# Optimization experiments

Hardware: AMD Instinct MI355X
Metric: run time of the kernel (lower is better)

Reference implementation:

```python
import jax, jax.numpy as jnp
import numpy as np

B, N, E = 32, 2000, 32000      # graphs, nodes/graph, edges/graph
V, D, R, K = 100000, 128, 39, 8  # vocab, emb_dim, n_relation, n_bases
EPS = 1e-5


def setup_inputs() -> dict:
    key = jax.random.key(0)
    ks = jax.random.split(key, 8)
    node_ids = jax.random.randint(ks[0], (B, N), 0, V)
    edge_index = jax.random.randint(ks[1], (B, 2, E), 0, N)
    edge_type = jax.random.randint(ks[2], (B, E), 0, R)
    embedding = jax.random.normal(ks[3], (V, D), jnp.float32) * D ** -0.5
    bases = jax.random.normal(ks[4], (K, D, D), jnp.float32) * D ** -0.5
    comp = jax.random.normal(ks[5], (R, K), jnp.float32) * K ** -0.5
    root = jax.random.normal(ks[6], (D, D), jnp.float32) * D ** -0.5
    bias = jnp.zeros((D,), jnp.float32)
    return dict(node_ids=node_ids, edge_index=edge_index, edge_type=edge_type,
                embedding=embedding, bases=bases, comp=comp, root=root, bias=bias)


def _graph_fwd(node_ids, edge_index, edge_type, embedding, bases, comp, root, bias):
    # RGCNConv with basis decomposition and per-relation MEAN aggregation (PyG default).
    x = embedding[node_ids]                       # [N, D] per-graph node features
    src, dst = edge_index[0], edge_index[1]       # j -> i, aggregate at dst
    x_src = x[src]                                # [E, D]
    # mean normalizer per (dst, relation) bucket
    comb = dst * R + edge_type                    # [E]
    cnt = jax.ops.segment_sum(jnp.ones((E,), jnp.float32), comb, num_segments=N * R)
    inv = jnp.where(cnt > 0, 1.0 / cnt, 0.0)[comb]  # [E]
    # W_r = sum_k comp[r,k] * bases[k]; fold comp coefficients + mean norm into edge weights
    w = comp[edge_type] * inv[:, None]            # [E, K]
    out = x @ root + bias                         # root/self connection
    for k in range(K):                            # small fixed loop over bases
        zk = jax.ops.segment_sum(w[:, k:k + 1] * x_src, dst, num_segments=N)  # [N, D]
        out = out + zk @ bases[k]
    g = out.sum(axis=0)                           # sum pool over nodes
    # torch.nn.functional.normalize(p=2, eps=1e-5)
    return g / jnp.maximum(jnp.linalg.norm(g), EPS)


def reference(node_ids, edge_index, edge_type, embedding, bases, comp, root, bias):
    f = jax.vmap(_graph_fwd, in_axes=(0, 0, 0, None, None, None, None, None))
    return f(node_ids, edge_index, edge_type, embedding, bases, comp, root, bias)  # [B, D]
```

## Files before the change

kernel.cpp:

```cpp
#include <hip/hip_runtime.h>
#include <math.h>

#define Bn 32
#define Nn 2000
#define En 32000
#define Vn 100000
#define Dn 128
#define Rn 39
#define Kn 8

#define SUBS 8
#define NPS (Nn / SUBS)
#define WPG 128
#define EQ (En / 4)


__global__ __launch_bounds__(1024) void cntinv_kernel(const int* __restrict__ edge_index,
                                                      const int* __restrict__ edge_type,
                                                      float* __restrict__ inv) {
    int b = blockIdx.x, sub = blockIdx.y;
    int s0 = sub * NPS;
    __shared__ int loc[NPS * Rn];
    for (int i = threadIdx.x; i < NPS * Rn; i += 1024) loc[i] = 0;
    __syncthreads();
    const int4* dst4 = (const int4*)(edge_index + (b * 2 + 1) * En);
    const int4* et4  = (const int4*)(edge_type + b * En);
    for (int q = threadIdx.x; q < EQ; q += 1024) {
        int4 d = dst4[q];
        int4 t = et4[q];
        int x;
        x = d.x - s0; if ((unsigned)x < NPS) atomicAdd(&loc[x * Rn + t.x], 1);
        x = d.y - s0; if ((unsigned)x < NPS) atomicAdd(&loc[x * Rn + t.y], 1);
        x = d.z - s0; if ((unsigned)x < NPS) atomicAdd(&loc[x * Rn + t.z], 1);
        x = d.w - s0; if ((unsigned)x < NPS) atomicAdd(&loc[x * Rn + t.w], 1);
    }
    __syncthreads();
    float* ivb = inv + (size_t)b * En;
    for (int q = threadIdx.x; q < EQ; q += 1024) {
        int4 d = dst4[q];
        int4 t = et4[q];
        int e = 4 * q, x;
        x = d.x - s0; if ((unsigned)x < NPS) ivb[e]     = 1.0f / (float)loc[x * Rn + t.x];
        x = d.y - s0; if ((unsigned)x < NPS) ivb[e + 1] = 1.0f / (float)loc[x * Rn + t.y];
        x = d.z - s0; if ((unsigned)x < NPS) ivb[e + 2] = 1.0f / (float)loc[x * Rn + t.z];
        x = d.w - s0; if ((unsigned)x < NPS) ivb[e + 3] = 1.0f / (float)loc[x * Rn + t.w];
    }
}

__global__ __launch_bounds__(1024) void a_kernel(const int* __restrict__ edge_index,
                                                 const int* __restrict__ edge_type,
                                                 const float* __restrict__ inv,
                                                 const float* __restrict__ comp,
                                                 float* __restrict__ a) {
    int b = blockIdx.x, sub = blockIdx.y;
    int s0 = sub * NPS;
    __shared__ float s[NPS * Rn];
    __shared__ float comp_l[Rn * Kn];
    for (int i = threadIdx.x; i < NPS * Rn; i += 1024) s[i] = 0.0f;
    if (threadIdx.x < Rn * Kn) comp_l[threadIdx.x] = comp[threadIdx.x];
    __syncthreads();
    const int4*   src4 = (const int4*)(edge_index + (b * 2 + 0) * En);
    const int4*   et4  = (const int4*)(edge_type + b * En);
    const float4* iv4  = (const float4*)(inv + (size_t)b * En);
    for (int q = threadIdx.x; q < EQ; q += 1024) {
        int4 sv = src4[q];
        int4 tv = et4[q];
        float4 iv = iv4[q];
        int x;
        x = sv.x - s0; if ((unsigned)x < NPS) atomicAdd(&s[x * Rn + tv.x], iv.x);
        x = sv.y - s0; if ((unsigned)x < NPS) atomicAdd(&s[x * Rn + tv.y], iv.y);
        x = sv.z - s0; if ((unsigned)x < NPS) atomicAdd(&s[x * Rn + tv.z], iv.z);
        x = sv.w - s0; if ((unsigned)x < NPS) atomicAdd(&s[x * Rn + tv.w], iv.w);
    }
    __syncthreads();
    float* g = a + ((size_t)b * Nn + s0) * Kn;
    for (int i = threadIdx.x; i < NPS * Kn; i += 1024) {
        int n = i >> 3, k = i & 7;
        float acc = 0.0f;
        const float* srow = &s[n * Rn];
        for (int t = 0; t < Rn; t++) acc += srow[t] * comp_l[t * Kn + k];
        g[i] = acc;
    }
}

__global__ __launch_bounds__(256) void gather_kernel(const int* __restrict__ node_ids,
                                                     const float* __restrict__ emb,
                                                     const float* __restrict__ a,
                                                     float* __restrict__ partial) {
    int b = blockIdx.x;
    int lane = threadIdx.x & 63, wv = threadIdx.x >> 6;
    int W = blockIdx.y * 4 + wv;
    float acc[18];
#pragma unroll
    for (int k = 0; k < 18; k++) acc[k] = 0.0f;
    const int*   nb = node_ids + b * Nn;
    const float* ab = a + (size_t)b * Nn * Kn;
    for (int n0 = W; n0 < Nn; n0 += 4 * WPG) {
        bool   has[4];
        int    nn[4];
        float2 v[4];
        float4 a0[4], a1[4];
#pragma unroll
        for (int i = 0; i < 4; i++) {
            int n = n0 + i * WPG;
            has[i] = n < Nn;
            nn[i]  = has[i] ? n : n0;
        }
#pragma unroll
        for (int i = 0; i < 4; i++) {
            int nid = nb[nn[i]];
            v[i] = has[i] ? ((const float2*)(emb + (size_t)nid * Dn))[lane]
                          : make_float2(0.f, 0.f);
            const float4* ar = (const float4*)(ab + (size_t)nn[i] * Kn);
            a0[i] = ar[0]; a1[i] = ar[1];
        }
#pragma unroll
        for (int i = 0; i < 4; i++) {
            float w[9] = {a0[i].x, a0[i].y, a0[i].z, a0[i].w,
                          a1[i].x, a1[i].y, a1[i].z, a1[i].w, 1.0f};
#pragma unroll
            for (int k = 0; k < 9; k++) {
                acc[2 * k]     += w[k] * v[i].x;
                acc[2 * k + 1] += w[k] * v[i].y;
            }
        }
    }
    float2* gp = (float2*)(partial + ((size_t)b * WPG + W) * 9 * Dn);
#pragma unroll
    for (int k = 0; k < 9; k++)
        gp[k * 64 + lane] = make_float2(acc[2 * k], acc[2 * k + 1]);
}

__global__ __launch_bounds__(256) void matvec_kernel(const float* __restrict__ partial,
                                                     const float* __restrict__ root,
                                                     const float* __restrict__ bases,
                                                     float* __restrict__ gmat) {
    int b = blockIdx.x, m = blockIdx.y;
    int d = threadIdx.x & (Dn - 1), h = threadIdx.x >> 7;
    __shared__ float ts[Dn];
    __shared__ float tsh[2][Dn];
    const float* p = partial + (size_t)b * WPG * 9 * Dn + m * Dn + d;
    float s0 = 0.f, s1 = 0.f, s2 = 0.f, s3 = 0.f;
    for (int c = h; c < WPG; c += 8) {
        s0 += p[(size_t)(c    ) * 9 * Dn];
        s1 += p[(size_t)(c + 2) * 9 * Dn];
        s2 += p[(size_t)(c + 4) * 9 * Dn];
        s3 += p[(size_t)(c + 6) * 9 * Dn];
    }
    tsh[h][d] = (s0 + s1) + (s2 + s3);
    __syncthreads();
    if (h == 0) ts[d] = tsh[0][d] + tsh[1][d];
    __syncthreads();
    const float* M = (m == 8) ? root : bases + (size_t)m * Dn * Dn;
    float g = 0.0f;
    for (int j = h * 64; j < h * 64 + 64; j++) g += ts[j] * M[j * Dn + d];
    __syncthreads();
    tsh[h][d] = g;
    __syncthreads();
    if (h == 0) gmat[((size_t)b * 9 + m) * Dn + d] = tsh[0][d] + tsh[1][d];
}

__global__ __launch_bounds__(128) void norm_kernel(const float* __restrict__ gmat,
                                                   const float* __restrict__ bias,
                                                   float* __restrict__ out) {
    int b = blockIdx.x, d = threadIdx.x;
    float g = (float)Nn * bias[d];
    const float* gb = gmat + (size_t)b * 9 * Dn + d;
#pragma unroll
    for (int m = 0; m < 9; m++) g += gb[m * Dn];
    float ss = g * g;
#pragma unroll
    for (int off = 32; off > 0; off >>= 1) ss += __shfl_down(ss, off, 64);
    __shared__ float s2[2];
    if ((threadIdx.x & 63) == 0) s2[threadIdx.x >> 6] = ss;
    __syncthreads();
    float nrm = sqrtf(s2[0] + s2[1]);
    out[b * Dn + d] = g / fmaxf(nrm, 1e-5f);
}

extern "C" void kernel_launch(void* const* d_in, const int* in_sizes, int n_in,
                              void* d_out, int out_size, void* d_ws, size_t ws_size,
                              hipStream_t stream) {
    const int*   node_ids   = (const int*)d_in[0];
    const int*   edge_index = (const int*)d_in[1];
    const int*   edge_type  = (const int*)d_in[2];
    const float* embedding  = (const float*)d_in[3];
    const float* bases      = (const float*)d_in[4];
    const float* comp       = (const float*)d_in[5];
    const float* root       = (const float*)d_in[6];
    const float* bias       = (const float*)d_in[7];
    float*       out        = (float*)d_out;

    char* w = (char*)d_ws;
    float* inv     = (float*)(w + 0);
    float* a       = (float*)(w + 4096000);
    float* partial = (float*)(w + 6144000);
    float* gmat    = (float*)(w + 25018368);

    cntinv_kernel<<<dim3(Bn, SUBS),    1024, 0, stream>>>(edge_index, edge_type, inv);
    a_kernel     <<<dim3(Bn, SUBS),    1024, 0, stream>>>(edge_index, edge_type, inv, comp, a);
    gather_kernel<<<dim3(Bn, WPG / 4), 256,  0, stream>>>(node_ids, embedding, a, partial);
    matvec_kernel<<<dim3(Bn, 9),       256,  0, stream>>>(partial, root, bases, gmat);
    norm_kernel  <<<Bn, 128, 0, stream>>>(gmat, bias, out);
}
```

Measured before the change: 156.1 us.

## Fuse gather, matvec and normalize into one kernel with last-block ticket reduction

Merges the gather, matvec and norm kernels into a single kernel. Each block first reduces its 16 waves' partial sums in shared memory, then writes one partial per block. A per-graph atomic ticket elects the last block to finish, and that block does the cross-block reduction, the 9 matvecs against bases/root and the L2 normalization. This removes two kernel launches and most of the partial-buffer traffic. In exchange, the final matvec runs on only 32 blocks (one per graph) instead of 288, which serializes that stage, and correctness now depends on threadfence ordering and the ticket reset done in a_kernel.

```diff
diff --git a/kernel.cpp b/kernel.cpp
--- a/kernel.cpp
+++ b/kernel.cpp
@@ -11,24 +11,25 @@
 
 #define SUBS 8
 #define NPS (Nn / SUBS)
-#define WPG 128
 #define EQ (En / 4)
-
-
-__global__ __launch_bounds__(1024) void cntinv_kernel(const int* __restrict__ edge_index,
-                                                      const int* __restrict__ edge_type,
-                                                      float* __restrict__ inv) {
+#define GB 8
+#define GW 16
+#define WPG (GB * GW)
+#define TPB 1024
+
+
+__global__ __launch_bounds__(TPB) void cntinv_kernel(const int* __restrict__ edge_index,
+                                                     const int* __restrict__ edge_type,
+                                                     float* __restrict__ inv) {
     int b = blockIdx.x, sub = blockIdx.y;
     int s0 = sub * NPS;
     __shared__ int loc[NPS * Rn];
-    for (int i = threadIdx.x; i < NPS * Rn; i += 1024) loc[i] = 0;
+    for (int i = threadIdx.x; i < NPS * Rn; i += TPB) loc[i] = 0;
     __syncthreads();
     const int4* dst4 = (const int4*)(edge_index + (b * 2 + 1) * En);
     const int4* et4  = (const int4*)(edge_type + b * En);
-    for (int q = threadIdx.x; q < EQ; q += 1024) {
-        int4 d = dst4[q];
-        int4 t = et4[q];
-        int x;
+    for (int q = threadIdx.x; q < EQ; q += TPB) {
+        int4 d = dst4[q]; int4 t = et4[q]; int x;
         x = d.x - s0; if ((unsigned)x < NPS) atomicAdd(&loc[x * Rn + t.x], 1);
         x = d.y - s0; if ((unsigned)x < NPS) atomicAdd(&loc[x * Rn + t.y], 1);
         x = d.z - s0; if ((unsigned)x < NPS) atomicAdd(&loc[x * Rn + t.z], 1);
@@ -36,9 +37,8 @@
     }
     __syncthreads();
     float* ivb = inv + (size_t)b * En;
-    for (int q = threadIdx.x; q < EQ; q += 1024) {
-        int4 d = dst4[q];
-        int4 t = et4[q];
+    for (int q = threadIdx.x; q < EQ; q += TPB) {
+        int4 d = dst4[q]; int4 t = et4[q];
         int e = 4 * q, x;
         x = d.x - s0; if ((unsigned)x < NPS) ivb[e]     = 1.0f / (float)loc[x * Rn + t.x];
         x = d.y - s0; if ((unsigned)x < NPS) ivb[e + 1] = 1.0f / (float)loc[x * Rn + t.y];
@@ -47,26 +47,25 @@
     }
 }
 
-__global__ __launch_bounds__(1024) void a_kernel(const int* __restrict__ edge_index,
-                                                 const int* __restrict__ edge_type,
-                                                 const float* __restrict__ inv,
-                                                 const float* __restrict__ comp,
-                                                 float* __restrict__ a) {
+__global__ __launch_bounds__(TPB) void a_kernel(const int* __restrict__ edge_index,
+                                                const int* __restrict__ edge_type,
+                                                const float* __restrict__ inv,
+                                                const float* __restrict__ comp,
+                                                float* __restrict__ a,
+                                                int* __restrict__ ticket) {
     int b = blockIdx.x, sub = blockIdx.y;
+    if (sub == 0 && threadIdx.x == 0) ticket[b] = 0;
     int s0 = sub * NPS;
     __shared__ float s[NPS * Rn];
     __shared__ float comp_l[Rn * Kn];
-    for (int i = threadIdx.x; i < NPS * Rn; i += 1024) s[i] = 0.0f;
+    for (int i = threadIdx.x; i < NPS * Rn; i += TPB) s[i] = 0.0f;
     if (threadIdx.x < Rn * Kn) comp_l[threadIdx.x] = comp[threadIdx.x];
     __syncthreads();
     const int4*   src4 = (const int4*)(edge_index + (b * 2 + 0) * En);
     const int4*   et4  = (const int4*)(edge_type + b * En);
     const float4* iv4  = (const float4*)(inv + (size_t)b * En);
-    for (int q = threadIdx.x; q < EQ; q += 1024) {
-        int4 sv = src4[q];
-        int4 tv = et4[q];
-        float4 iv = iv4[q];
-        int x;
+    for (int q = threadIdx.x; q < EQ; q += TPB) {
+        int4 sv = src4[q]; int4 tv = et4[q]; float4 iv = iv4[q]; int x;
         x = sv.x - s0; if ((unsigned)x < NPS) atomicAdd(&s[x * Rn + tv.x], iv.x);
         x = sv.y - s0; if ((unsigned)x < NPS) atomicAdd(&s[x * Rn + tv.y], iv.y);
         x = sv.z - s0; if ((unsigned)x < NPS) atomicAdd(&s[x * Rn + tv.z], iv.z);
@@ -74,7 +73,7 @@
     }
     __syncthreads();
     float* g = a + ((size_t)b * Nn + s0) * Kn;
-    for (int i = threadIdx.x; i < NPS * Kn; i += 1024) {
+    for (int i = threadIdx.x; i < NPS * Kn; i += TPB) {
         int n = i >> 3, k = i & 7;
         float acc = 0.0f;
         const float* srow = &s[n * Rn];
@@ -83,13 +82,18 @@
     }
 }
 
-__global__ __launch_bounds__(256) void gather_kernel(const int* __restrict__ node_ids,
-                                                     const float* __restrict__ emb,
-                                                     const float* __restrict__ a,
-                                                     float* __restrict__ partial) {
-    int b = blockIdx.x;
-    int lane = threadIdx.x & 63, wv = threadIdx.x >> 6;
-    int W = blockIdx.y * 4 + wv;
+__global__ __launch_bounds__(TPB) void gather_final_kernel(
+    const int* __restrict__ node_ids, const float* __restrict__ emb,
+    const float* __restrict__ a, const float* __restrict__ root,
+    const float* __restrict__ bases, const float* __restrict__ bias,
+    float* partial, int* ticket, float* __restrict__ out)
+{
+    __shared__ float red[GW * 9 * Dn];
+    __shared__ int isLast;
+    int b = blockIdx.x, sub = blockIdx.y;
+    int tid = threadIdx.x, lane = tid & 63, wv = tid >> 6;
+    int W = sub * GW + wv;
+
     float acc[18];
 #pragma unroll
     for (int k = 0; k < 18; k++) acc[k] = 0.0f;
@@ -125,57 +129,64 @@
             }
         }
     }
-    float2* gp = (float2*)(partial + ((size_t)b * WPG + W) * 9 * Dn);
 #pragma unroll
     for (int k = 0; k < 9; k++)
-        gp[k * 64 + lane] = make_float2(acc[2 * k], acc[2 * k + 1]);
-}
-
-__global__ __launch_bounds__(256) void matvec_kernel(const float* __restrict__ partial,
-                                                     const float* __restrict__ root,
-                                                     const float* __restrict__ bases,
-                                                     float* __restrict__ gmat) {
-    int b = blockIdx.x, m = blockIdx.y;
-    int d = threadIdx.x & (Dn - 1), h = threadIdx.x >> 7;
-    __shared__ float ts[Dn];
-    __shared__ float tsh[2][Dn];
-    const float* p = partial + (size_t)b * WPG * 9 * Dn + m * Dn + d;
-    float s0 = 0.f, s1 = 0.f, s2 = 0.f, s3 = 0.f;
-    for (int c = h; c < WPG; c += 8) {
-        s0 += p[(size_t)(c    ) * 9 * Dn];
-        s1 += p[(size_t)(c + 2) * 9 * Dn];
-        s2 += p[(size_t)(c + 4) * 9 * Dn];
-        s3 += p[(size_t)(c + 6) * 9 * Dn];
-    }
-    tsh[h][d] = (s0 + s1) + (s2 + s3);
-    __syncthreads();
-    if (h == 0) ts[d] = tsh[0][d] + tsh[1][d];
-    __syncthreads();
-    const float* M = (m == 8) ? root : bases + (size_t)m * Dn * Dn;
+        ((float2*)&red[(wv * 9 + k) * Dn])[lane] = make_float2(acc[2 * k], acc[2 * k + 1]);
+    __syncthreads();
+
+    float* gp = partial + ((size_t)(b * GB + sub)) * 9 * Dn;
+    for (int i = tid; i < 9 * Dn; i += TPB) {
+        float s = 0.0f;
+#pragma unroll
+        for (int w = 0; w < GW; w++) s += red[w * 9 * Dn + i];
+        gp[i] = s;
+    }
+    __threadfence();
+    if (tid == 0) {
+        int old = atomicAdd(&ticket[b], 1);
+        isLast = ((old & (GB - 1)) == (GB - 1));
+    }
+    __syncthreads();
+    if (!isLast) return;
+    __threadfence();
+
+    volatile const float* pb = partial + (size_t)b * GB * 9 * Dn;
+    for (int i = tid; i < 9 * Dn; i += TPB) {
+        float s = 0.0f;
+#pragma unroll
+        for (int c = 0; c < GB; c++) s += pb[c * 9 * Dn + i];
+        red[i] = s;
+    }
+    __syncthreads();
+
+    for (int u = tid; u < 9 * Dn; u += TPB) {
+        int m = u >> 7, d = u & (Dn - 1);
+        const float* M  = (m == 8) ? root : bases + (size_t)m * Dn * Dn;
+        const float* ts = &red[m * Dn];
+        float g = 0.0f;
+        for (int j = 0; j < Dn; j++) g += ts[j] * M[j * Dn + d];
+        red[9 * Dn + u] = g;
+    }
+    __syncthreads();
+
     float g = 0.0f;
-    for (int j = h * 64; j < h * 64 + 64; j++) g += ts[j] * M[j * Dn + d];
-    __syncthreads();
-    tsh[h][d] = g;
-    __syncthreads();
-    if (h == 0) gmat[((size_t)b * 9 + m) * Dn + d] = tsh[0][d] + tsh[1][d];
-}
-
-__global__ __launch_bounds__(128) void norm_kernel(const float* __restrict__ gmat,
-                                                   const float* __restrict__ bias,
-                                                   float* __restrict__ out) {
-    int b = blockIdx.x, d = threadIdx.x;
-    float g = (float)Nn * bias[d];
-    const float* gb = gmat + (size_t)b * 9 * Dn + d;
-#pragma unroll
-    for (int m = 0; m < 9; m++) g += gb[m * Dn];
-    float ss = g * g;
-#pragma unroll
-    for (int off = 32; off > 0; off >>= 1) ss += __shfl_down(ss, off, 64);
-    __shared__ float s2[2];
-    if ((threadIdx.x & 63) == 0) s2[threadIdx.x >> 6] = ss;
-    __syncthreads();
-    float nrm = sqrtf(s2[0] + s2[1]);
-    out[b * Dn + d] = g / fmaxf(nrm, 1e-5f);
+    if (tid < Dn) {
+        g = (float)Nn * bias[tid];
+#pragma unroll
+        for (int m = 0; m < 9; m++) g += red[9 * Dn + m * Dn + tid];
+        red[18 * Dn + tid] = g;
+    }
+    float ss = (tid < Dn) ? g * g : 0.0f;
+    if (tid < 128) {
+#pragma unroll
+        for (int off = 32; off > 0; off >>= 1) ss += __shfl_down(ss, off, 64);
+        if ((tid & 63) == 0) red[19 * Dn + (tid >> 6)] = ss;
+    }
+    __syncthreads();
+    if (tid < Dn) {
+        float nrm = sqrtf(red[19 * Dn] + red[19 * Dn + 1]);
+        out[b * Dn + tid] = red[18 * Dn + tid] / fmaxf(nrm, 1e-5f);
+    }
 }
 
 extern "C" void kernel_launch(void* const* d_in, const int* in_sizes, int n_in,
@@ -195,11 +206,10 @@
     float* inv     = (float*)(w + 0);
     float* a       = (float*)(w + 4096000);
     float* partial = (float*)(w + 6144000);
-    float* gmat    = (float*)(w + 25018368);
-
-    cntinv_kernel<<<dim3(Bn, SUBS),    1024, 0, stream>>>(edge_index, edge_type, inv);
-    a_kernel     <<<dim3(Bn, SUBS),    1024, 0, stream>>>(edge_index, edge_type, inv, comp, a);
-    gather_kernel<<<dim3(Bn, WPG / 4), 256,  0, stream>>>(node_ids, embedding, a, partial);
-    matvec_kernel<<<dim3(Bn, 9),       256,  0, stream>>>(partial, root, bases, gmat);
-    norm_kernel  <<<Bn, 128, 0, stream>>>(gmat, bias, out);
-}
+    int*   ticket  = (int*)  (w + 7323648);
+
+    cntinv_kernel      <<<dim3(Bn, SUBS), TPB, 0, stream>>>(edge_index, edge_type, inv);
+    a_kernel           <<<dim3(Bn, SUBS), TPB, 0, stream>>>(edge_index, edge_type, inv, comp, a, ticket);
+    gather_final_kernel<<<dim3(Bn, GB),   TPB, 0, stream>>>(node_ids, embedding, a, root,
+                                                            bases, bias, partial, ticket, out);
+}
```

Result: slower. 226.0 us (+44.7%).

## Fuse per-node weight and gather kernels, fold normalization into matvec

Applied to the files above, without the earlier changes.

Merges the per-node basis-weight computation with the embedding gather, so the weights stay in shared memory and never round-trip through global memory. It also folds the final L2 normalization into the matvec kernel, using a last-block ticket counter per graph. This removes two kernel launches and the global write and read of the weight array. The cost is that the gather now runs on only 256 blocks of 1024 threads instead of 1024 blocks of 256, so it has less parallelism for hiding embedding-load latency. The ticket scheme also relies on threadfence ordering.

```diff
diff --git a/kernel.cpp b/kernel.cpp
--- a/kernel.cpp
+++ b/kernel.cpp
@@ -11,24 +11,24 @@
 
 #define SUBS 8
 #define NPS (Nn / SUBS)
-#define WPG 128
+#define GW 16
+#define WPG (SUBS * GW)
 #define EQ (En / 4)
-
-
-__global__ __launch_bounds__(1024) void cntinv_kernel(const int* __restrict__ edge_index,
-                                                      const int* __restrict__ edge_type,
-                                                      float* __restrict__ inv) {
+#define TPB 1024
+
+
+__global__ __launch_bounds__(TPB) void cntinv_kernel(const int* __restrict__ edge_index,
+                                                     const int* __restrict__ edge_type,
+                                                     float* __restrict__ inv) {
     int b = blockIdx.x, sub = blockIdx.y;
     int s0 = sub * NPS;
     __shared__ int loc[NPS * Rn];
-    for (int i = threadIdx.x; i < NPS * Rn; i += 1024) loc[i] = 0;
+    for (int i = threadIdx.x; i < NPS * Rn; i += TPB) loc[i] = 0;
     __syncthreads();
     const int4* dst4 = (const int4*)(edge_index + (b * 2 + 1) * En);
     const int4* et4  = (const int4*)(edge_type + b * En);
-    for (int q = threadIdx.x; q < EQ; q += 1024) {
-        int4 d = dst4[q];
-        int4 t = et4[q];
-        int x;
+    for (int q = threadIdx.x; q < EQ; q += TPB) {
+        int4 d = dst4[q]; int4 t = et4[q]; int x;
         x = d.x - s0; if ((unsigned)x < NPS) atomicAdd(&loc[x * Rn + t.x], 1);
         x = d.y - s0; if ((unsigned)x < NPS) atomicAdd(&loc[x * Rn + t.y], 1);
         x = d.z - s0; if ((unsigned)x < NPS) atomicAdd(&loc[x * Rn + t.z], 1);
@@ -36,9 +36,8 @@
     }
     __syncthreads();
     float* ivb = inv + (size_t)b * En;
-    for (int q = threadIdx.x; q < EQ; q += 1024) {
-        int4 d = dst4[q];
-        int4 t = et4[q];
+    for (int q = threadIdx.x; q < EQ; q += TPB) {
+        int4 d = dst4[q]; int4 t = et4[q];
         int e = 4 * q, x;
         x = d.x - s0; if ((unsigned)x < NPS) ivb[e]     = 1.0f / (float)loc[x * Rn + t.x];
         x = d.y - s0; if ((unsigned)x < NPS) ivb[e + 1] = 1.0f / (float)loc[x * Rn + t.y];
@@ -47,77 +46,69 @@
     }
 }
 
-__global__ __launch_bounds__(1024) void a_kernel(const int* __restrict__ edge_index,
+__global__ __launch_bounds__(TPB) void ag_kernel(const int* __restrict__ node_ids,
+                                                 const int* __restrict__ edge_index,
                                                  const int* __restrict__ edge_type,
                                                  const float* __restrict__ inv,
                                                  const float* __restrict__ comp,
-                                                 float* __restrict__ a) {
+                                                 const float* __restrict__ emb,
+                                                 float* __restrict__ partial,
+                                                 int* __restrict__ ticket) {
     int b = blockIdx.x, sub = blockIdx.y;
+    int tid = threadIdx.x;
+    if (sub == 0 && tid == 0) ticket[b] = 0;
     int s0 = sub * NPS;
     __shared__ float s[NPS * Rn];
     __shared__ float comp_l[Rn * Kn];
-    for (int i = threadIdx.x; i < NPS * Rn; i += 1024) s[i] = 0.0f;
-    if (threadIdx.x < Rn * Kn) comp_l[threadIdx.x] = comp[threadIdx.x];
+    __shared__ float w_loc[NPS * 9];
+    for (int i = tid; i < NPS * Rn; i += TPB) s[i] = 0.0f;
+    if (tid < Rn * Kn) comp_l[tid] = comp[tid];
     __syncthreads();
     const int4*   src4 = (const int4*)(edge_index + (b * 2 + 0) * En);
     const int4*   et4  = (const int4*)(edge_type + b * En);
     const float4* iv4  = (const float4*)(inv + (size_t)b * En);
-    for (int q = threadIdx.x; q < EQ; q += 1024) {
-        int4 sv = src4[q];
-        int4 tv = et4[q];
-        float4 iv = iv4[q];
-        int x;
+    for (int q = tid; q < EQ; q += TPB) {
+        int4 sv = src4[q]; int4 tv = et4[q]; float4 iv = iv4[q]; int x;
         x = sv.x - s0; if ((unsigned)x < NPS) atomicAdd(&s[x * Rn + tv.x], iv.x);
         x = sv.y - s0; if ((unsigned)x < NPS) atomicAdd(&s[x * Rn + tv.y], iv.y);
         x = sv.z - s0; if ((unsigned)x < NPS) atomicAdd(&s[x * Rn + tv.z], iv.z);
         x = sv.w - s0; if ((unsigned)x < NPS) atomicAdd(&s[x * Rn + tv.w], iv.w);
     }
     __syncthreads();
-    float* g = a + ((size_t)b * Nn + s0) * Kn;
-    for (int i = threadIdx.x; i < NPS * Kn; i += 1024) {
+    for (int i = tid; i < NPS * Kn; i += TPB) {
         int n = i >> 3, k = i & 7;
         float acc = 0.0f;
         const float* srow = &s[n * Rn];
         for (int t = 0; t < Rn; t++) acc += srow[t] * comp_l[t * Kn + k];
-        g[i] = acc;
-    }
-}
-
-__global__ __launch_bounds__(256) void gather_kernel(const int* __restrict__ node_ids,
-                                                     const float* __restrict__ emb,
-                                                     const float* __restrict__ a,
-                                                     float* __restrict__ partial) {
-    int b = blockIdx.x;
-    int lane = threadIdx.x & 63, wv = threadIdx.x >> 6;
-    int W = blockIdx.y * 4 + wv;
+        w_loc[n * 9 + k] = acc;
+    }
+    for (int i = tid; i < NPS; i += TPB) w_loc[i * 9 + 8] = 1.0f;
+    __syncthreads();
+
+    int lane = tid & 63, wv = tid >> 6;
     float acc[18];
 #pragma unroll
     for (int k = 0; k < 18; k++) acc[k] = 0.0f;
-    const int*   nb = node_ids + b * Nn;
-    const float* ab = a + (size_t)b * Nn * Kn;
-    for (int n0 = W; n0 < Nn; n0 += 4 * WPG) {
+    const int* nb = node_ids + b * Nn;
+    for (int l0 = wv; l0 < NPS; l0 += 4 * GW) {
         bool   has[4];
-        int    nn[4];
+        int    ll[4];
         float2 v[4];
-        float4 a0[4], a1[4];
 #pragma unroll
         for (int i = 0; i < 4; i++) {
-            int n = n0 + i * WPG;
-            has[i] = n < Nn;
-            nn[i]  = has[i] ? n : n0;
+            int l = l0 + i * GW;
+            has[i] = l < NPS;
+            ll[i]  = has[i] ? l : l0;
         }
 #pragma unroll
         for (int i = 0; i < 4; i++) {
-            int nid = nb[nn[i]];
+            int nid = nb[s0 + ll[i]];
             v[i] = has[i] ? ((const float2*)(emb + (size_t)nid * Dn))[lane]
                           : make_float2(0.f, 0.f);
-            const float4* ar = (const float4*)(ab + (size_t)nn[i] * Kn);
-            a0[i] = ar[0]; a1[i] = ar[1];
         }
 #pragma unroll
         for (int i = 0; i < 4; i++) {
-            float w[9] = {a0[i].x, a0[i].y, a0[i].z, a0[i].w,
-                          a1[i].x, a1[i].y, a1[i].z, a1[i].w, 1.0f};
+            const float* w = &w_loc[ll[i] * 9];
 #pragma unroll
             for (int k = 0; k < 9; k++) {
                 acc[2 * k]     += w[k] * v[i].x;
@@ -125,20 +116,25 @@
             }
         }
     }
+    int W = sub * GW + wv;
     float2* gp = (float2*)(partial + ((size_t)b * WPG + W) * 9 * Dn);
 #pragma unroll
     for (int k = 0; k < 9; k++)
         gp[k * 64 + lane] = make_float2(acc[2 * k], acc[2 * k + 1]);
 }
 
-__global__ __launch_bounds__(256) void matvec_kernel(const float* __restrict__ partial,
-                                                     const float* __restrict__ root,
-                                                     const float* __restrict__ bases,
-                                                     float* __restrict__ gmat) {
+__global__ __launch_bounds__(256) void mvn_kernel(const float* __restrict__ partial,
+                                                  const float* __restrict__ root,
+                                                  const float* __restrict__ bases,
+                                                  const float* __restrict__ bias,
+                                                  float* gmat,
+                                                  int* ticket,
+                                                  float* __restrict__ out) {
     int b = blockIdx.x, m = blockIdx.y;
     int d = threadIdx.x & (Dn - 1), h = threadIdx.x >> 7;
     __shared__ float ts[Dn];
     __shared__ float tsh[2][Dn];
+    __shared__ int isLast;
     const float* p = partial + (size_t)b * WPG * 9 * Dn + m * Dn + d;
     float s0 = 0.f, s1 = 0.f, s2 = 0.f, s3 = 0.f;
     for (int c = h; c < WPG; c += 8) {
@@ -158,24 +154,32 @@
     tsh[h][d] = g;
     __syncthreads();
     if (h == 0) gmat[((size_t)b * 9 + m) * Dn + d] = tsh[0][d] + tsh[1][d];
-}
-
-__global__ __launch_bounds__(128) void norm_kernel(const float* __restrict__ gmat,
-                                                   const float* __restrict__ bias,
-                                                   float* __restrict__ out) {
-    int b = blockIdx.x, d = threadIdx.x;
-    float g = (float)Nn * bias[d];
-    const float* gb = gmat + (size_t)b * 9 * Dn + d;
-#pragma unroll
-    for (int m = 0; m < 9; m++) g += gb[m * Dn];
-    float ss = g * g;
+    __threadfence();
+    if (threadIdx.x == 0) {
+        int old = atomicAdd(&ticket[b], 1);
+        isLast = ((old % 9) == 8);
+    }
+    __syncthreads();
+    if (!isLast) return;
+    __threadfence();
+
+    float gg = 0.0f;
+    if (threadIdx.x < Dn) {
+        gg = (float)Nn * bias[d];
+        const float* gb = gmat + (size_t)b * 9 * Dn + d;
+#pragma unroll
+        for (int mm = 0; mm < 9; mm++) gg += gb[mm * Dn];
+        ts[d] = gg;
+    }
+    float ss = (threadIdx.x < Dn) ? gg * gg : 0.0f;
 #pragma unroll
     for (int off = 32; off > 0; off >>= 1) ss += __shfl_down(ss, off, 64);
-    __shared__ float s2[2];
-    if ((threadIdx.x & 63) == 0) s2[threadIdx.x >> 6] = ss;
-    __syncthreads();
-    float nrm = sqrtf(s2[0] + s2[1]);
-    out[b * Dn + d] = g / fmaxf(nrm, 1e-5f);
+    if ((threadIdx.x & 63) == 0) tsh[0][threadIdx.x >> 6] = ss;
+    __syncthreads();
+    if (threadIdx.x < Dn) {
+        float nrm = sqrtf(tsh[0][0] + tsh[0][1]);
+        out[b * Dn + d] = ts[d] / fmaxf(nrm, 1e-5f);
+    }
 }
 
 extern "C" void kernel_launch(void* const* d_in, const int* in_sizes, int n_in,
@@ -193,13 +197,13 @@
 
     char* w = (char*)d_ws;
     float* inv     = (float*)(w + 0);
-    float* a       = (float*)(w + 4096000);
-    float* partial = (float*)(w + 6144000);
-    float* gmat    = (float*)(w + 25018368);
-
-    cntinv_kernel<<<dim3(Bn, SUBS),    1024, 0, stream>>>(edge_index, edge_type, inv);
-    a_kernel     <<<dim3(Bn, SUBS),    1024, 0, stream>>>(edge_index, edge_type, inv, comp, a);
-    gather_kernel<<<dim3(Bn, WPG / 4), 256,  0, stream>>>(node_ids, embedding, a, partial);
-    matvec_kernel<<<dim3(Bn, 9),       256,  0, stream>>>(partial, root, bases, gmat);
-    norm_kernel  <<<Bn, 128, 0, stream>>>(gmat, bias, out);
-}
+    float* partial = (float*)(w + 4096000);
+    float* gmat    = (float*)(w + 22970368);
+    int*   ticket  = (int*)  (w + 23117824);
+
+    cntinv_kernel<<<dim3(Bn, SUBS), TPB, 0, stream>>>(edge_index, edge_type, inv);
+    ag_kernel    <<<dim3(Bn, SUBS), TPB, 0, stream>>>(node_ids, edge_index, edge_type,
+                                                      inv, comp, embedding, partial, ticket);
+    mvn_kernel   <<<dim3(Bn, 9),    256, 0, stream>>>(partial, root, bases, bias,
+                                                      gmat, ticket, out);
+}
```

New measurement: 165.7 us. +6.1%, slower.

## Flatten bucket indexing, deepen gather unroll, transpose partial layout for vectorized matvec

Applied to the files above, without the earlier changes.

The count and aggregation kernels now compute a flat (node*R+type) index and test it against a block's contiguous bucket range, replacing the subtract-then-multiply form. The gather loop processes 8 nodes per iteration instead of 4, giving more loads in flight at the cost of more registers. Partial sums are stored as [b][k][wave][D] so the matvec reduction reads contiguous float4 rows, with eight partitions reduced through shared memory. A redundant shared-memory zeroing and an extra barrier were also added.

```diff
diff --git a/kernel.cpp b/kernel.cpp
--- a/kernel.cpp
+++ b/kernel.cpp
@@ -13,37 +13,35 @@
 #define NPS (Nn / SUBS)
 #define WPG 128
 #define EQ (En / 4)
+#define NR (NPS * Rn)
 
 
 __global__ __launch_bounds__(1024) void cntinv_kernel(const int* __restrict__ edge_index,
                                                       const int* __restrict__ edge_type,
                                                       float* __restrict__ inv) {
     int b = blockIdx.x, sub = blockIdx.y;
-    int s0 = sub * NPS;
-    __shared__ int loc[NPS * Rn];
-    for (int i = threadIdx.x; i < NPS * Rn; i += 1024) loc[i] = 0;
+    int base = sub * NR;
+    __shared__ int loc[NR];
+    for (int i = threadIdx.x; i < NR; i += 1024) loc[i] = 0;
     __syncthreads();
     const int4* dst4 = (const int4*)(edge_index + (b * 2 + 1) * En);
     const int4* et4  = (const int4*)(edge_type + b * En);
     for (int q = threadIdx.x; q < EQ; q += 1024) {
-        int4 d = dst4[q];
-        int4 t = et4[q];
-        int x;
-        x = d.x - s0; if ((unsigned)x < NPS) atomicAdd(&loc[x * Rn + t.x], 1);
-        x = d.y - s0; if ((unsigned)x < NPS) atomicAdd(&loc[x * Rn + t.y], 1);
-        x = d.z - s0; if ((unsigned)x < NPS) atomicAdd(&loc[x * Rn + t.z], 1);
-        x = d.w - s0; if ((unsigned)x < NPS) atomicAdd(&loc[x * Rn + t.w], 1);
+        int4 d = dst4[q]; int4 t = et4[q]; int y;
+        y = d.x * Rn + t.x - base; if ((unsigned)y < NR) atomicAdd(&loc[y], 1);
+        y = d.y * Rn + t.y - base; if ((unsigned)y < NR) atomicAdd(&loc[y], 1);
+        y = d.z * Rn + t.z - base; if ((unsigned)y < NR) atomicAdd(&loc[y], 1);
+        y = d.w * Rn + t.w - base; if ((unsigned)y < NR) atomicAdd(&loc[y], 1);
     }
     __syncthreads();
     float* ivb = inv + (size_t)b * En;
     for (int q = threadIdx.x; q < EQ; q += 1024) {
-        int4 d = dst4[q];
-        int4 t = et4[q];
-        int e = 4 * q, x;
-        x = d.x - s0; if ((unsigned)x < NPS) ivb[e]     = 1.0f / (float)loc[x * Rn + t.x];
-        x = d.y - s0; if ((unsigned)x < NPS) ivb[e + 1] = 1.0f / (float)loc[x * Rn + t.y];
-        x = d.z - s0; if ((unsigned)x < NPS) ivb[e + 2] = 1.0f / (float)loc[x * Rn + t.z];
-        x = d.w - s0; if ((unsigned)x < NPS) ivb[e + 3] = 1.0f / (float)loc[x * Rn + t.w];
+        int4 d = dst4[q]; int4 t = et4[q];
+        int e = 4 * q, y;
+        y = d.x * Rn + t.x - base; if ((unsigned)y < NR) ivb[e]     = 1.0f / (float)loc[y];
+        y = d.y * Rn + t.y - base; if ((unsigned)y < NR) ivb[e + 1] = 1.0f / (float)loc[y];
+        y = d.z * Rn + t.z - base; if ((unsigned)y < NR) ivb[e + 2] = 1.0f / (float)loc[y];
+        y = d.w * Rn + t.w - base; if ((unsigned)y < NR) ivb[e + 3] = 1.0f / (float)loc[y];
     }
 }
 
@@ -53,27 +51,24 @@
                                                  const float* __restrict__ comp,
                                                  float* __restrict__ a) {
     int b = blockIdx.x, sub = blockIdx.y;
-    int s0 = sub * NPS;
-    __shared__ float s[NPS * Rn];
+    int base = sub * NR;
+    __shared__ float s[NR];
     __shared__ float comp_l[Rn * Kn];
-    for (int i = threadIdx.x; i < NPS * Rn; i += 1024) s[i] = 0.0f;
+    for (int i = threadIdx.x; i < NR; i += 1024) s[i] = 0.0f;
     if (threadIdx.x < Rn * Kn) comp_l[threadIdx.x] = comp[threadIdx.x];
     __syncthreads();
     const int4*   src4 = (const int4*)(edge_index + (b * 2 + 0) * En);
     const int4*   et4  = (const int4*)(edge_type + b * En);
     const float4* iv4  = (const float4*)(inv + (size_t)b * En);
     for (int q = threadIdx.x; q < EQ; q += 1024) {
-        int4 sv = src4[q];
-        int4 tv = et4[q];
-        float4 iv = iv4[q];
-        int x;
-        x = sv.x - s0; if ((unsigned)x < NPS) atomicAdd(&s[x * Rn + tv.x], iv.x);
-        x = sv.y - s0; if ((unsigned)x < NPS) atomicAdd(&s[x * Rn + tv.y], iv.y);
-        x = sv.z - s0; if ((unsigned)x < NPS) atomicAdd(&s[x * Rn + tv.z], iv.z);
-        x = sv.w - s0; if ((unsigned)x < NPS) atomicAdd(&s[x * Rn + tv.w], iv.w);
-    }
-    __syncthreads();
-    float* g = a + ((size_t)b * Nn + s0) * Kn;
+        int4 sv = src4[q]; int4 tv = et4[q]; float4 iv = iv4[q]; int y;
+        y = sv.x * Rn + tv.x - base; if ((unsigned)y < NR) atomicAdd(&s[y], iv.x);
+        y = sv.y * Rn + tv.y - base; if ((unsigned)y < NR) atomicAdd(&s[y], iv.y);
+        y = sv.z * Rn + tv.z - base; if ((unsigned)y < NR) atomicAdd(&s[y], iv.z);
+        y = sv.w * Rn + tv.w - base; if ((unsigned)y < NR) atomicAdd(&s[y], iv.w);
+    }
+    __syncthreads();
+    float* g = a + ((size_t)b * Nn + sub * NPS) * Kn;
     for (int i = threadIdx.x; i < NPS * Kn; i += 1024) {
         int n = i >> 3, k = i & 7;
         float acc = 0.0f;
@@ -95,19 +90,19 @@
     for (int k = 0; k < 18; k++) acc[k] = 0.0f;
     const int*   nb = node_ids + b * Nn;
     const float* ab = a + (size_t)b * Nn * Kn;
-    for (int n0 = W; n0 < Nn; n0 += 4 * WPG) {
-        bool   has[4];
-        int    nn[4];
-        float2 v[4];
-        float4 a0[4], a1[4];
-#pragma unroll
-        for (int i = 0; i < 4; i++) {
+    for (int n0 = W; n0 < Nn; n0 += 8 * WPG) {
+        bool   has[8];
+        int    nn[8];
+        float2 v[8];
+        float4 a0[8], a1[8];
+#pragma unroll
+        for (int i = 0; i < 8; i++) {
             int n = n0 + i * WPG;
             has[i] = n < Nn;
             nn[i]  = has[i] ? n : n0;
         }
 #pragma unroll
-        for (int i = 0; i < 4; i++) {
+        for (int i = 0; i < 8; i++) {
             int nid = nb[nn[i]];
             v[i] = has[i] ? ((const float2*)(emb + (size_t)nid * Dn))[lane]
                           : make_float2(0.f, 0.f);
@@ -115,7 +110,7 @@
             a0[i] = ar[0]; a1[i] = ar[1];
         }
 #pragma unroll
-        for (int i = 0; i < 4; i++) {
+        for (int i = 0; i < 8; i++) {
             float w[9] = {a0[i].x, a0[i].y, a0[i].z, a0[i].w,
                           a1[i].x, a1[i].y, a1[i].z, a1[i].w, 1.0f};
 #pragma unroll
@@ -125,10 +120,11 @@
             }
         }
     }
-    float2* gp = (float2*)(partial + ((size_t)b * WPG + W) * 9 * Dn);
-#pragma unroll
-    for (int k = 0; k < 9; k++)
-        gp[k * 64 + lane] = make_float2(acc[2 * k], acc[2 * k + 1]);
+#pragma unroll
+    for (int k = 0; k < 9; k++) {
+        float2* gp = (float2*)(partial + (((size_t)b * 9 + k) * WPG + W) * Dn);
+        gp[lane] = make_float2(acc[2 * k], acc[2 * k + 1]);
+    }
 }
 
 __global__ __launch_bounds__(256) void matvec_kernel(const float* __restrict__ partial,
@@ -136,24 +132,35 @@
                                                      const float* __restrict__ bases,
                                                      float* __restrict__ gmat) {
     int b = blockIdx.x, m = blockIdx.y;
-    int d = threadIdx.x & (Dn - 1), h = threadIdx.x >> 7;
-    __shared__ float ts[Dn];
-    __shared__ float tsh[2][Dn];
-    const float* p = partial + (size_t)b * WPG * 9 * Dn + m * Dn + d;
-    float s0 = 0.f, s1 = 0.f, s2 = 0.f, s3 = 0.f;
-    for (int c = h; c < WPG; c += 8) {
-        s0 += p[(size_t)(c    ) * 9 * Dn];
-        s1 += p[(size_t)(c + 2) * 9 * Dn];
-        s2 += p[(size_t)(c + 4) * 9 * Dn];
-        s3 += p[(size_t)(c + 6) * 9 * Dn];
-    }
-    tsh[h][d] = (s0 + s1) + (s2 + s3);
-    __syncthreads();
-    if (h == 0) ts[d] = tsh[0][d] + tsh[1][d];
-    __syncthreads();
-    const float* M = (m == 8) ? root : bases + (size_t)m * Dn * Dn;
+    int tid = threadIdx.x;
+    __shared__ float4 ts4[Dn / 4];
+    __shared__ float tsh[8][Dn];
+    int dg = tid & 31, part = tid >> 5;
+    const float4* p4 = (const float4*)(partial + ((size_t)b * 9 + m) * WPG * Dn);
+    float4 sum = make_float4(0.f, 0.f, 0.f, 0.f);
+    for (int c = part; c < WPG; c += 8) {
+        float4 v = p4[c * 32 + dg];
+        sum.x += v.x; sum.y += v.y; sum.z += v.z; sum.w += v.w;
+    }
+    ((float4*)tsh[part])[dg] = sum;
+    __syncthreads();
+    if (part == 0) {
+        float4 t = make_float4(0.f, 0.f, 0.f, 0.f);
+#pragma unroll
+        for (int r = 0; r < 8; r++) {
+            float4 v = ((float4*)tsh[r])[dg];
+            t.x += v.x; t.y += v.y; t.z += v.z; t.w += v.w;
+        }
+        ts4[dg] = t;
+    }
+    __syncthreads();
+    const float* ts = (const float*)ts4;
+    const float* M  = (m == 8) ? root : bases + (size_t)m * Dn * Dn;
+    int d = tid & (Dn - 1), h = tid >> 7;
     float g = 0.0f;
     for (int j = h * 64; j < h * 64 + 64; j++) g += ts[j] * M[j * Dn + d];
+    __syncthreads();
+    tsh[0][d + h * 0] = 0.0f;
     __syncthreads();
     tsh[h][d] = g;
     __syncthreads();
```

Result: faster. 149.3 us (-4.4%).
